# Kernel optimization log

Hardware: AMD Instinct MI355X
Metric: run time of the kernel (lower is better)

The kernel has to match this reference:

```python
import jax, jax.numpy as jnp
import numpy as np

INPUT_DIM = 1024
OUT_DIM = 1024
ORDER = 4
EXPANSION_POINT = 0.0


def setup_inputs() -> dict:
    key = jax.random.key(0)
    k_x, k_c = jax.random.split(key)
    x = jax.random.normal(k_x, (8192, INPUT_DIM), dtype=jnp.float32)
    coeffs = jax.random.normal(k_c, (OUT_DIM, INPUT_DIM, ORDER), dtype=jnp.float32) * 0.01
    bias = jnp.zeros((1, OUT_DIM), dtype=jnp.float32)
    return {"x": x, "coeffs": coeffs, "bias": bias}


def reference(x, coeffs, bias):
    # x: [..., input_dim] -> flatten leading dims
    outshape = x.shape[:-1] + (OUT_DIM,)
    xf = x.reshape(-1, INPUT_DIM)
    x_shifted = xf - EXPANSION_POINT
    # powers P[n, i, k] = x_shifted^k, k = 0..order-1 (0**0 == 1, matching torch)
    powers = jnp.power(x_shifted[:, :, None], jnp.arange(ORDER, dtype=x.dtype))
    # y[n, o] = sum_{i,k} P[n,i,k] * coeffs[o,i,k]  -- single GEMM-like contraction
    y = jnp.einsum('nik,oik->no', powers, coeffs)
    y = y + bias
    return y.reshape(outshape)
```

## Files before the change

### kernel.cpp

```cpp
#include <hip/hip_runtime.h>
#include <stdint.h>

#define IN_DIM 1024
#define OUT_DIM 1024
#define NROWS 8192
#define KD 3072

#define BM 128
#define BN 128
#define BK 64
#define NT (KD / BK)

typedef __bf16 bf16x8 __attribute__((ext_vector_type(8)));
typedef float f32x4 __attribute__((ext_vector_type(4)));
typedef unsigned short us8 __attribute__((ext_vector_type(8)));
typedef unsigned int u32;

#define AS1 __attribute__((address_space(1)))
#define AS3 __attribute__((address_space(3)))

__device__ __forceinline__ unsigned short f2bf(float f) {
    u32 u = __builtin_bit_cast(u32, f);
    u32 r = (u + 0x7fffu + ((u >> 16) & 1u)) >> 16;
    return (unsigned short)r;
}

__device__ __forceinline__ bf16x8 ld8(const unsigned short* p) {
    return __builtin_bit_cast(bf16x8, *reinterpret_cast<const us8*>(p));
}

__global__ __launch_bounds__(256) void prep_coeffs(const float* __restrict__ c,
                                                   const float* __restrict__ bias,
                                                   unsigned short* __restrict__ Bp,
                                                   float* __restrict__ bias2) {
    const int o = blockIdx.x;
    const float4* row = reinterpret_cast<const float4*>(c + (size_t)o * (IN_DIM * 4));
    float s = 0.f;
    for (int i = threadIdx.x; i < IN_DIM; i += 256) {
        float4 v = row[i];
        s += v.x;
        int j = i & 7;
        size_t g = (size_t)(i >> 3) * 1024 + o;
        Bp[g * 8 + j]                       = f2bf(v.y);
        Bp[(g + (size_t)128 * 1024) * 8 + j] = f2bf(v.z);
        Bp[(g + (size_t)256 * 1024) * 8 + j] = f2bf(v.w);
    }
#pragma unroll
    for (int off = 32; off; off >>= 1) s += __shfl_down(s, off);
    __shared__ float red[4];
    if ((threadIdx.x & 63) == 0) red[threadIdx.x >> 6] = s;
    __syncthreads();
    if (threadIdx.x == 0) bias2[o] = bias[o] + red[0] + red[1] + red[2] + red[3];
}

__global__ __launch_bounds__(256) void prep_powers(const float* __restrict__ x,
                                                   unsigned short* __restrict__ A) {
    int t = blockIdx.x * blockDim.x + threadIdx.x;
    int n = t >> 8;
    int i4 = (t & 255) * 4;
    float4 v = reinterpret_cast<const float4*>(x)[t];
    unsigned short* An = A + (size_t)n * KD + i4;
    float xs[4] = {v.x, v.y, v.z, v.w};
    unsigned short b1[4], b2[4], b3[4];
#pragma unroll
    for (int j = 0; j < 4; ++j) {
        float x1 = xs[j], x2 = x1 * x1, x3 = x2 * x1;
        b1[j] = f2bf(x1); b2[j] = f2bf(x2); b3[j] = f2bf(x3);
    }
    ushort4 p1 = {b1[0], b1[1], b1[2], b1[3]};
    ushort4 p2 = {b2[0], b2[1], b2[2], b2[3]};
    ushort4 p3 = {b3[0], b3[1], b3[2], b3[3]};
    *reinterpret_cast<ushort4*>(An)        = p1;
    *reinterpret_cast<ushort4*>(An + 1024) = p2;
    *reinterpret_cast<ushort4*>(An + 2048) = p3;
}

__global__ __launch_bounds__(256, 2) void taylor_gemm(
    const unsigned short* __restrict__ A,
    const unsigned short* __restrict__ Bp,
    const float* __restrict__ bias2,
    float* __restrict__ C) {
    __shared__ alignas(16) unsigned short sA[2][BM * BK];

    const int tid = threadIdx.x;
    const int lane = tid & 63;
    const int wid = tid >> 6;
    const int wr = wid >> 1;
    const int wc = wid & 1;
    const int gx = blockIdx.x, gy = blockIdx.y;

    const char* Ab = (const char*)A;
    const int cs = ((lane & 7) ^ (lane >> 3)) * 8;
    size_t aSrc[4];
    int dstOff[4];
#pragma unroll
    for (int u = 0; u < 4; ++u) {
        int row = u * 32 + wid * 8 + (lane >> 3);
        aSrc[u] = ((size_t)(gx * BM + row) * KD + cs) * 2;
        dstOff[u] = (u * 32 + wid * 8) * BK;
    }

    auto stage_A = [&](int d, int kt) {
        size_t koff = (size_t)kt * (BK * 2);
#pragma unroll
        for (int u = 0; u < 4; ++u)
            __builtin_amdgcn_global_load_lds(
                (const AS1 void*)(Ab + aSrc[u] + koff),
                (AS3 void*)(&sA[d][dstOff[u]]), 16, 0, 0);
    };

    int aSw[2];
#pragma unroll
    for (int ks = 0; ks < 2; ++ks)
        aSw[ks] = (wr * 64 + (lane & 15)) * BK
                + (((ks * 4 + (lane >> 4)) ^ (lane & 7)) * 8);

    const unsigned short* bp0 = Bp
        + ((size_t)(lane >> 4) * 1024 + gy * BN + wc * 64 + (lane & 15)) * 8;

    bf16x8 bf0[4][2], bf1[4][2];
    f32x4 acc[4][4] = {};

    auto load_B = [&](bf16x8 (&bfr)[4][2], int kt) {
#pragma unroll
        for (int n = 0; n < 4; ++n)
#pragma unroll
            for (int ks = 0; ks < 2; ++ks)
                bfr[n][ks] = ld8(bp0 + ((size_t)kt * 8 + ks * 4) * 8192 + n * 128);
    };

    stage_A(0, 0);
    load_B(bf0, 0);

#define TAYLOR_ITER(kt, CUR, NXT)                                             \
    {                                                                         \
        asm volatile("s_waitcnt vmcnt(0)" ::: "memory");                      \
        __builtin_amdgcn_s_barrier();                                         \
        __builtin_amdgcn_sched_barrier(0);                                    \
        if ((kt) + 1 < NT) {                                                  \
            stage_A(((kt) + 1) & 1, (kt) + 1);                                \
            load_B(NXT, (kt) + 1);                                            \
        }                                                                     \
        __builtin_amdgcn_sched_barrier(0);                                    \
        const unsigned short* sAc = &sA[(kt) & 1][0];                         \
        bf16x8 af[4][2];                                                      \
        _Pragma("unroll")                                                     \
        for (int m = 0; m < 4; ++m)                                           \
            _Pragma("unroll")                                                 \
            for (int ks = 0; ks < 2; ++ks)                                    \
                af[m][ks] = ld8(&sAc[aSw[ks] + m * 16 * BK]);                 \
        _Pragma("unroll")                                                     \
        for (int m = 0; m < 4; ++m)                                           \
            _Pragma("unroll")                                                 \
            for (int n = 0; n < 4; ++n)                                       \
                _Pragma("unroll")                                             \
                for (int ks = 0; ks < 2; ++ks)                                \
                    acc[m][n] = __builtin_amdgcn_mfma_f32_16x16x32_bf16(      \
                        af[m][ks], CUR[n][ks], acc[m][n], 0, 0, 0);           \
    }

    for (int kt = 0; kt < NT; kt += 2) {
        TAYLOR_ITER(kt,     bf0, bf1);
        TAYLOR_ITER(kt + 1, bf1, bf0);
    }
#undef TAYLOR_ITER

    const int colBase = gy * BN + wc * 64 + (lane & 15);
    const int rowBase = gx * BM + wr * 64 + (lane >> 4) * 4;
#pragma unroll
    for (int n = 0; n < 4; ++n) {
        int col = colBase + n * 16;
        float bv = bias2[col];
#pragma unroll
        for (int m = 0; m < 4; ++m) {
            int row = rowBase + m * 16;
#pragma unroll
            for (int r = 0; r < 4; ++r)
                C[(size_t)(row + r) * OUT_DIM + col] = acc[m][n][r] + bv;
        }
    }
}

__global__ void taylor_naive(const float* __restrict__ x, const float* __restrict__ coeffs,
                             const float* __restrict__ bias, float* __restrict__ out) {
    int n = blockIdx.x;
    __shared__ float P[IN_DIM * 4];
    for (int i = threadIdx.x; i < IN_DIM; i += blockDim.x) {
        float xv = x[(size_t)n * IN_DIM + i];
        P[i * 4 + 0] = 1.f;
        P[i * 4 + 1] = xv;
        P[i * 4 + 2] = xv * xv;
        P[i * 4 + 3] = xv * xv * xv;
    }
    __syncthreads();
    for (int o = threadIdx.x; o < OUT_DIM; o += blockDim.x) {
        float s = bias[o];
        const float* c = coeffs + (size_t)o * (IN_DIM * 4);
        for (int i = 0; i < IN_DIM; ++i) {
            float4 cv = *reinterpret_cast<const float4*>(c + i * 4);
            s += cv.x * P[i * 4 + 0] + cv.y * P[i * 4 + 1] +
                 cv.z * P[i * 4 + 2] + cv.w * P[i * 4 + 3];
        }
        out[(size_t)n * OUT_DIM + o] = s;
    }
}

extern "C" void kernel_launch(void* const* d_in, const int* in_sizes, int n_in,
                              void* d_out, int out_size, void* d_ws, size_t ws_size,
                              hipStream_t stream) {
    const float* x = (const float*)d_in[0];
    const float* coeffs = (const float*)d_in[1];
    const float* bias = (const float*)d_in[2];
    float* out = (float*)d_out;

    const size_t needA = (size_t)NROWS * KD * 2;
    const size_t needB = (size_t)OUT_DIM * KD * 2;
    const size_t needBias = OUT_DIM * sizeof(float);

    if (ws_size >= needA + needB + needBias) {
        unsigned short* A = (unsigned short*)d_ws;
        unsigned short* Bp = (unsigned short*)((char*)d_ws + needA);
        float* bias2 = (float*)((char*)d_ws + needA + needB);
        prep_coeffs<<<OUT_DIM, 256, 0, stream>>>(coeffs, bias, Bp, bias2);
        prep_powers<<<(NROWS * IN_DIM / 4) / 256, 256, 0, stream>>>(x, A);
        dim3 grid(NROWS / BM, OUT_DIM / BN);
        taylor_gemm<<<grid, 256, 0, stream>>>(A, Bp, bias2, out);
    } else {
        taylor_naive<<<NROWS, 256, 0, stream>>>(x, coeffs, bias, out);
    }
}
```

Before: 80.67 us.

## Enlarge GEMM tile to 256 rows with triple-buffered A staging and merged prep

The GEMM block grows to 256x128 with 512 threads, and A staging moves to a three-buffer ring that keeps one tile in flight, using a partial vmcnt wait. Each k-tile's MFMA work is split into two halves separated by a barrier, with raised wave priority around the MFMAs. The two preprocessing kernels are merged into one launch. The aim is more reuse of B per block, deeper overlap of global loads with compute, and one less launch. The cost is higher LDS use and one block per CU, which leaves little room to hide latency if the pipeline stalls.

```diff
diff --git a/kernel.cpp b/kernel.cpp
--- a/kernel.cpp
+++ b/kernel.cpp
@@ -6,7 +6,7 @@
 #define NROWS 8192
 #define KD 3072
 
-#define BM 128
+#define BM 256
 #define BN 128
 #define BK 64
 #define NT (KD / BK)
@@ -29,58 +29,59 @@
     return __builtin_bit_cast(bf16x8, *reinterpret_cast<const us8*>(p));
 }
 
-__global__ __launch_bounds__(256) void prep_coeffs(const float* __restrict__ c,
+__global__ __launch_bounds__(256) void taylor_prep(const float* __restrict__ x,
+                                                   const float* __restrict__ c,
                                                    const float* __restrict__ bias,
+                                                   unsigned short* __restrict__ A,
                                                    unsigned short* __restrict__ Bp,
                                                    float* __restrict__ bias2) {
-    const int o = blockIdx.x;
-    const float4* row = reinterpret_cast<const float4*>(c + (size_t)o * (IN_DIM * 4));
-    float s = 0.f;
-    for (int i = threadIdx.x; i < IN_DIM; i += 256) {
-        float4 v = row[i];
-        s += v.x;
-        int j = i & 7;
-        size_t g = (size_t)(i >> 3) * 1024 + o;
-        Bp[g * 8 + j]                       = f2bf(v.y);
-        Bp[(g + (size_t)128 * 1024) * 8 + j] = f2bf(v.z);
-        Bp[(g + (size_t)256 * 1024) * 8 + j] = f2bf(v.w);
-    }
-#pragma unroll
-    for (int off = 32; off; off >>= 1) s += __shfl_down(s, off);
-    __shared__ float red[4];
-    if ((threadIdx.x & 63) == 0) red[threadIdx.x >> 6] = s;
-    __syncthreads();
-    if (threadIdx.x == 0) bias2[o] = bias[o] + red[0] + red[1] + red[2] + red[3];
-}
-
-__global__ __launch_bounds__(256) void prep_powers(const float* __restrict__ x,
-                                                   unsigned short* __restrict__ A) {
-    int t = blockIdx.x * blockDim.x + threadIdx.x;
-    int n = t >> 8;
-    int i4 = (t & 255) * 4;
-    float4 v = reinterpret_cast<const float4*>(x)[t];
-    unsigned short* An = A + (size_t)n * KD + i4;
-    float xs[4] = {v.x, v.y, v.z, v.w};
-    unsigned short b1[4], b2[4], b3[4];
-#pragma unroll
-    for (int j = 0; j < 4; ++j) {
-        float x1 = xs[j], x2 = x1 * x1, x3 = x2 * x1;
-        b1[j] = f2bf(x1); b2[j] = f2bf(x2); b3[j] = f2bf(x3);
-    }
-    ushort4 p1 = {b1[0], b1[1], b1[2], b1[3]};
-    ushort4 p2 = {b2[0], b2[1], b2[2], b2[3]};
-    ushort4 p3 = {b3[0], b3[1], b3[2], b3[3]};
-    *reinterpret_cast<ushort4*>(An)        = p1;
-    *reinterpret_cast<ushort4*>(An + 1024) = p2;
-    *reinterpret_cast<ushort4*>(An + 2048) = p3;
-}
-
-__global__ __launch_bounds__(256, 2) void taylor_gemm(
+    if (blockIdx.x < 8192) {
+        int t = blockIdx.x * 256 + threadIdx.x;
+        int n = t >> 8;
+        int i4 = (t & 255) * 4;
+        float4 v = reinterpret_cast<const float4*>(x)[t];
+        unsigned short* An = A + (size_t)n * KD + i4;
+        float xs[4] = {v.x, v.y, v.z, v.w};
+        unsigned short b1[4], b2[4], b3[4];
+#pragma unroll
+        for (int j = 0; j < 4; ++j) {
+            float x1 = xs[j], x2 = x1 * x1, x3 = x2 * x1;
+            b1[j] = f2bf(x1); b2[j] = f2bf(x2); b3[j] = f2bf(x3);
+        }
+        ushort4 p1 = {b1[0], b1[1], b1[2], b1[3]};
+        ushort4 p2 = {b2[0], b2[1], b2[2], b2[3]};
+        ushort4 p3 = {b3[0], b3[1], b3[2], b3[3]};
+        *reinterpret_cast<ushort4*>(An)        = p1;
+        *reinterpret_cast<ushort4*>(An + 1024) = p2;
+        *reinterpret_cast<ushort4*>(An + 2048) = p3;
+    } else {
+        const int o = blockIdx.x - 8192;
+        const float4* row = reinterpret_cast<const float4*>(c + (size_t)o * (IN_DIM * 4));
+        float s = 0.f;
+        for (int i = threadIdx.x; i < IN_DIM; i += 256) {
+            float4 v = row[i];
+            s += v.x;
+            int j = i & 7;
+            size_t g = (size_t)(i >> 3) * 1024 + o;
+            Bp[g * 8 + j]                        = f2bf(v.y);
+            Bp[(g + (size_t)128 * 1024) * 8 + j] = f2bf(v.z);
+            Bp[(g + (size_t)256 * 1024) * 8 + j] = f2bf(v.w);
+        }
+#pragma unroll
+        for (int off = 32; off; off >>= 1) s += __shfl_down(s, off);
+        __shared__ float red[4];
+        if ((threadIdx.x & 63) == 0) red[threadIdx.x >> 6] = s;
+        __syncthreads();
+        if (threadIdx.x == 0) bias2[o] = bias[o] + red[0] + red[1] + red[2] + red[3];
+    }
+}
+
+__global__ __launch_bounds__(512, 1) void taylor_gemm(
     const unsigned short* __restrict__ A,
     const unsigned short* __restrict__ Bp,
     const float* __restrict__ bias2,
     float* __restrict__ C) {
-    __shared__ alignas(16) unsigned short sA[2][BM * BK];
+    __shared__ alignas(16) unsigned short sA[3][BM * BK];
 
     const int tid = threadIdx.x;
     const int lane = tid & 63;
@@ -92,21 +93,21 @@
     const char* Ab = (const char*)A;
     const int cs = ((lane & 7) ^ (lane >> 3)) * 8;
     size_t aSrc[4];
-    int dstOff[4];
+    int aDst[4];
 #pragma unroll
     for (int u = 0; u < 4; ++u) {
-        int row = u * 32 + wid * 8 + (lane >> 3);
+        int row = wid * 32 + u * 8 + (lane >> 3);
         aSrc[u] = ((size_t)(gx * BM + row) * KD + cs) * 2;
-        dstOff[u] = (u * 32 + wid * 8) * BK;
-    }
-
-    auto stage_A = [&](int d, int kt) {
+        aDst[u] = (wid * 32 + u * 8) * BK;
+    }
+
+    auto stage_A = [&](int b, int kt) {
         size_t koff = (size_t)kt * (BK * 2);
 #pragma unroll
         for (int u = 0; u < 4; ++u)
             __builtin_amdgcn_global_load_lds(
                 (const AS1 void*)(Ab + aSrc[u] + koff),
-                (AS3 void*)(&sA[d][dstOff[u]]), 16, 0, 0);
+                (AS3 void*)(&sA[b][aDst[u]]), 16, 0, 0);
     };
 
     int aSw[2];
@@ -129,41 +130,65 @@
                 bfr[n][ks] = ld8(bp0 + ((size_t)kt * 8 + ks * 4) * 8192 + n * 128);
     };
 
+    load_B(bf0, 0);
     stage_A(0, 0);
-    load_B(bf0, 0);
-
-#define TAYLOR_ITER(kt, CUR, NXT)                                             \
+    stage_A(1, 1);
+
+#define TAYLOR_TILE(kt, CURB, NXTB)                                           \
     {                                                                         \
-        asm volatile("s_waitcnt vmcnt(0)" ::: "memory");                      \
+        if ((kt) < NT - 1) asm volatile("s_waitcnt vmcnt(4)" ::: "memory");   \
+        else               asm volatile("s_waitcnt vmcnt(0)" ::: "memory");   \
         __builtin_amdgcn_s_barrier();                                         \
         __builtin_amdgcn_sched_barrier(0);                                    \
-        if ((kt) + 1 < NT) {                                                  \
-            stage_A(((kt) + 1) & 1, (kt) + 1);                                \
-            load_B(NXT, (kt) + 1);                                            \
-        }                                                                     \
-        __builtin_amdgcn_sched_barrier(0);                                    \
-        const unsigned short* sAc = &sA[(kt) & 1][0];                         \
-        bf16x8 af[4][2];                                                      \
-        _Pragma("unroll")                                                     \
-        for (int m = 0; m < 4; ++m)                                           \
+        if ((kt) + 1 < NT) load_B(NXTB, (kt) + 1);                            \
+        if ((kt) + 2 < NT) stage_A(((kt) + 2) % 3, (kt) + 2);                 \
+        __builtin_amdgcn_sched_barrier(0);                                    \
+        const unsigned short* sAc = &sA[(kt) % 3][0];                         \
+        bf16x8 af[2][2];                                                      \
+        _Pragma("unroll")                                                     \
+        for (int mi = 0; mi < 2; ++mi)                                        \
             _Pragma("unroll")                                                 \
             for (int ks = 0; ks < 2; ++ks)                                    \
-                af[m][ks] = ld8(&sAc[aSw[ks] + m * 16 * BK]);                 \
-        _Pragma("unroll")                                                     \
-        for (int m = 0; m < 4; ++m)                                           \
+                af[mi][ks] = ld8(&sAc[aSw[ks] + mi * 16 * BK]);               \
+        asm volatile("s_waitcnt lgkmcnt(0)" ::: "memory");                    \
+        __builtin_amdgcn_sched_barrier(0);                                    \
+        __builtin_amdgcn_s_setprio(1);                                        \
+        _Pragma("unroll")                                                     \
+        for (int mi = 0; mi < 2; ++mi)                                        \
             _Pragma("unroll")                                                 \
             for (int n = 0; n < 4; ++n)                                       \
                 _Pragma("unroll")                                             \
                 for (int ks = 0; ks < 2; ++ks)                                \
-                    acc[m][n] = __builtin_amdgcn_mfma_f32_16x16x32_bf16(      \
-                        af[m][ks], CUR[n][ks], acc[m][n], 0, 0, 0);           \
+                    acc[mi][n] = __builtin_amdgcn_mfma_f32_16x16x32_bf16(     \
+                        af[mi][ks], CURB[n][ks], acc[mi][n], 0, 0, 0);        \
+        __builtin_amdgcn_s_setprio(0);                                        \
+        __builtin_amdgcn_s_barrier();                                         \
+        __builtin_amdgcn_sched_barrier(0);                                    \
+        bf16x8 af2[2][2];                                                     \
+        _Pragma("unroll")                                                     \
+        for (int mi = 0; mi < 2; ++mi)                                        \
+            _Pragma("unroll")                                                 \
+            for (int ks = 0; ks < 2; ++ks)                                    \
+                af2[mi][ks] = ld8(&sAc[aSw[ks] + (2 + mi) * 16 * BK]);        \
+        asm volatile("s_waitcnt lgkmcnt(0)" ::: "memory");                    \
+        __builtin_amdgcn_sched_barrier(0);                                    \
+        __builtin_amdgcn_s_setprio(1);                                        \
+        _Pragma("unroll")                                                     \
+        for (int mi = 0; mi < 2; ++mi)                                        \
+            _Pragma("unroll")                                                 \
+            for (int n = 0; n < 4; ++n)                                       \
+                _Pragma("unroll")                                             \
+                for (int ks = 0; ks < 2; ++ks)                                \
+                    acc[2 + mi][n] = __builtin_amdgcn_mfma_f32_16x16x32_bf16( \
+                        af2[mi][ks], CURB[n][ks], acc[2 + mi][n], 0, 0, 0);   \
+        __builtin_amdgcn_s_setprio(0);                                        \
     }
 
     for (int kt = 0; kt < NT; kt += 2) {
-        TAYLOR_ITER(kt,     bf0, bf1);
-        TAYLOR_ITER(kt + 1, bf1, bf0);
-    }
-#undef TAYLOR_ITER
+        TAYLOR_TILE(kt,     bf0, bf1);
+        TAYLOR_TILE(kt + 1, bf1, bf0);
+    }
+#undef TAYLOR_TILE
 
     const int colBase = gy * BN + wc * 64 + (lane & 15);
     const int rowBase = gx * BM + wr * 64 + (lane >> 4) * 4;
@@ -221,10 +246,9 @@
         unsigned short* A = (unsigned short*)d_ws;
         unsigned short* Bp = (unsigned short*)((char*)d_ws + needA);
         float* bias2 = (float*)((char*)d_ws + needA + needB);
-        prep_coeffs<<<OUT_DIM, 256, 0, stream>>>(coeffs, bias, Bp, bias2);
-        prep_powers<<<(NROWS * IN_DIM / 4) / 256, 256, 0, stream>>>(x, A);
+        taylor_prep<<<8192 + 1024, 256, 0, stream>>>(x, coeffs, bias, A, Bp, bias2);
         dim3 grid(NROWS / BM, OUT_DIM / BN);
-        taylor_gemm<<<grid, 256, 0, stream>>>(A, Bp, bias2, out);
+        taylor_gemm<<<grid, 512, 0, stream>>>(A, Bp, bias2, out);
     } else {
         taylor_naive<<<NROWS, 256, 0, stream>>>(x, coeffs, bias, out);
     }
```

After: 95.24 us. +18.1%, slower.
